# Optimization experiments

Measured on AMD Instinct MI355X. Metric: run time of the kernel, lower is better.

The kernel has to match this reference:

```python
import jax, jax.numpy as jnp
import numpy as np

TAPS, DIMS, SPS = 32, 2, 2
LR_W, LR_F, LR_S, LR_B = 1.0 / 2**6, 1.0 / 2**7, 0.0, 1.0 / 2**11
GRAD_MAX_W, GRAD_MAX_F = 30.0, 30.0
EPS, BETA = 1e-8, 0.0


def _const16qam():
    # commplax comm.const('16QAM', norm=True): unit-average-power 16QAM grid
    p = np.array([-3.0, -1.0, 1.0, 3.0], dtype=np.float32)
    c = (p[:, None] + 1j * p[None, :]).reshape(-1) / np.sqrt(10.0)
    return jnp.asarray(c, dtype=jnp.complex64)


def _frame(x, flen, fstep):
    # xop.frame: [L, D] -> [(L-flen)//fstep + 1, flen, D]
    n = (x.shape[0] - flen) // fstep + 1
    idx = jnp.arange(n)[:, None] * fstep + jnp.arange(flen)[None, :]
    return x[idx]


def _clip(g, gmax):
    # same math as jnp.where(|g|>gmax, g/|g|*gmax, g), but NaN-safe under AD
    ag = jnp.abs(g)
    return g * jnp.minimum(1.0, gmax / jnp.maximum(ag, 1e-30))


def _ddlms(x):
    const = _const16qam()
    u_all = _frame(x, TAPS, SPS)  # [N, taps, dims] complex64

    def step(state, u):
        w, f, s, b, fshat = state
        v = jnp.einsum('ijt,tj->i', w, u)          # mimo filter output [dims]
        k = v * f
        c = k * s
        z = c + b
        q = v * fshat + b
        # decision-directed symbol (train=False, no truth)
        d = const[jnp.argmin(jnp.abs(const[:, None] - q[None, :]), axis=0)]
        psi_hat = jnp.abs(f) / f * jnp.abs(s) / s
        e_w = (d - b) * psi_hat - v
        e_f = d - b - k
        e_s = d - b - c
        e_b = d - z
        gw = -1.0 / ((jnp.abs(u) ** 2).sum() + EPS) * e_w[:, None, None] * u.conj().T[None, ...]
        gf = -1.0 / (jnp.abs(v) ** 2 + EPS) * e_f * v.conj()
        gs = -1.0 / (jnp.abs(k) ** 2 + EPS) * e_s * k.conj()
        gb = -e_b
        gw = _clip(gw, GRAD_MAX_W)
        gf = _clip(gf, GRAD_MAX_F)
        out = (w, f, s, b)  # pre-update params are used by apply
        wn = w - LR_W * gw
        fn = f - LR_F * gf
        sn = s - LR_S * gs
        bn = b - LR_B * gb
        fshatn = BETA * fshat + (1.0 - BETA) * (fn * sn)
        return (wn, fn, sn, bn, fshatn), out

    dt = jnp.complex64
    state0 = (jnp.zeros((DIMS, DIMS, TAPS), dt),   # w0 (mimoinit='zeros')
              jnp.ones((DIMS,), dt),               # f0
              jnp.ones((DIMS,), dt),               # s0
              jnp.zeros((DIMS,), dt),              # b0
              jnp.ones((DIMS,), dt))               # fshat0
    _, (ws, fs, ss, bs) = jax.lax.scan(step, state0, u_all)
    # mimo_apply: vmap(mimo)(ws, u_all) * fs * ss + bs
    y = jnp.einsum('nijt,ntj->ni', ws, u_all) * fs * ss + bs  # [N, dims]
    return y


def setup_inputs() -> dict:
    key = jax.random.key(0)
    k1, k2 = jax.random.split(key)
    x_re = jax.random.normal(k1, (200000, 2), dtype=jnp.float32)
    x_im = jax.random.normal(k2, (200000, 2), dtype=jnp.float32)
    return {"x_re": x_re, "x_im": x_im}


def reference(x_re, x_im):
    x = jax.lax.complex(x_re, x_im)  # [2N, 2] complex64
    y = _ddlms(x)                    # [(2N-taps)//sps + 1, 2] complex64
    return jnp.stack([y.real, y.imag], axis=-1)  # [N_out, 2, 2] float32
```

## Files before the change

### kernel.cpp

```cpp
#include <hip/hip_runtime.h>

typedef unsigned u2v __attribute__((ext_vector_type(2)));

template<int CTRL>
__device__ __forceinline__ float dpp_xadd(float v) {
    int s = __builtin_amdgcn_update_dpp(0, __float_as_int(v), CTRL, 0xF, 0xF, true);
    return v + __int_as_float(s);
}

#if __has_builtin(__builtin_amdgcn_permlane16_swap)
__device__ __forceinline__ float xor16_add(float v) {
    u2v r = __builtin_amdgcn_permlane16_swap((unsigned)__float_as_int(v),
                                             (unsigned)__float_as_int(v),
                                             false, false);
    return __int_as_float((int)r.x) + __int_as_float((int)r.y);
}
#else
__device__ __forceinline__ float xor16_add(float v) {
    int s = __builtin_amdgcn_ds_swizzle(__float_as_int(v), 0x401F);
    return v + __int_as_float(s);
}
#endif

__device__ __forceinline__ float red32(float v) {
    v = dpp_xadd<0xB1>(v);
    v = dpp_xadd<0x4E>(v);
    v = dpp_xadd<0x141>(v);
    v = dpp_xadd<0x140>(v);
    v = xor16_add(v);
    return v;
}

__global__ void pre_tab(const float* __restrict__ xre,
                        const float* __restrict__ xim,
                        float4* __restrict__ tab, int ns) {
    int n = blockIdx.x * blockDim.x + threadIdx.x;
    if (n >= ns) return;
    const float* ar = xre + 4 * n;
    const float* ai = xim + 4 * n;
    float un = 0.f;
    #pragma unroll 8
    for (int k = 0; k < 64; ++k) un = fmaf(ar[k], ar[k], fmaf(ai[k], ai[k], un));
    float s = (1.0f / 64.0f) / (un + 1e-8f);
    float cr = 0.f, ci = 0.f;
    if (n + 1 < ns) {
        const float* br_ = ar + 4;
        const float* bi_ = ai + 4;
        #pragma unroll 8
        for (int k = 0; k < 64; ++k) {
            cr = fmaf(ar[k], br_[k], fmaf(ai[k], bi_[k], cr));
            ci = fmaf(ar[k], bi_[k], ci);
            ci = fmaf(-ai[k], br_[k], ci);
        }
    }
    tab[n] = make_float4(s, s * cr, s * ci, 0.f);
}

#define NSTEPS 99985

__global__ __launch_bounds__(128, 1)
void ddlms_scan2(const float* __restrict__ xre,
                 const float* __restrict__ xim,
                 const float4* __restrict__ tab,
                 float* __restrict__ out) {
    const int tid = (int)threadIdx.x;
    const int wid = tid >> 6;
    const int l = tid & 63;
    const int m = l & 31;
    const int half = l >> 5;

    constexpr float EPSv = 1e-8f;
    constexpr float LRF  = 1.0f / 128.0f;
    constexpr float LRB  = 1.0f / 2048.0f;
    const float B1 = 0.6324555320336759f;
    const float A1 = 0.31622776601683794f;
    const float A3 = 0.9486832980505138f;

    __shared__ float2 sh[8];
    if (tid < 8) sh[tid] = make_float2(0.f, 0.f);
    __syncthreads();

    float2* __restrict__ o2 = reinterpret_cast<float2*>(out);

    if (wid == 0) {
        float fr = 1.f, fi = 0.f, br = 0.f, bi = 0.f, psr = 1.f, psj = 0.f;
        float ewPr = 0.f, ewPi = 0.f, sCPr = 0.f, sCPi = 0.f;
        float4 t0 = tab[0], t1 = tab[1], t2 = tab[2], t3;

        auto W0 = [&](int n, int P, float4& tC, float4& tF) {
            __syncthreads();
            float2 bas = sh[2 * P + half];
            float Dr = fmaf(ewPr, sCPr, -(ewPi * sCPi));
            float Di = fmaf(ewPr, sCPi,   ewPi * sCPr);
            float vr = bas.x + Dr, vi = bas.y + Di;
            { int nn = n + 3; if (nn > NSTEPS - 1) nn = NSTEPS - 1; tF = tab[nn]; }

            float kr = fmaf(vr, fr, -(vi * fi));
            float ki = fmaf(vr, fi,   vi * fr);
            float zr = kr + br, zi = ki + bi;
            if (m == 0) o2[2 * n + half] = make_float2(zr, zi);

            float magr = (fabsf(zr) > B1) ? A3 : A1;
            float dr   = (zr <= 0.f) ? -magr : magr;
            float magi = (fabsf(zi) > B1) ? A3 : A1;
            float di   = (zi <= 0.f) ? -magi : magi;

            float er = dr - zr, ei = di - zi;

            float v2  = fmaf(vr, vr, fmaf(vi, vi, EPSv));
            float rv  = __builtin_amdgcn_rcpf(v2);
            float gfr = fmaf(er, vr,   ei * vi)  * rv;
            float gfi = fmaf(ei, vr, -(er * vi)) * rv;
            float m2  = fmaf(gfr, gfr, gfi * gfi);
            float scf = fminf(1.f, 30.f * __builtin_amdgcn_rsqf(m2));
            float tf  = LRF * scf;

            float dbr = dr - br, dbi = di - bi;
            float ewr = fmaf(dbr, psr, -(dbi * psj)) - vr;
            float ewi = fmaf(dbr, psj,   dbi * psr)  - vi;

            float ewsr = tC.x * ewr, ewsi = tC.x * ewi;
            if (m == 0) sh[4 + 2 * P + half] = make_float2(ewsr, ewsi);

            fr = fmaf(tf, gfr, fr); fi = fmaf(tf, gfi, fi);
            br = fmaf(LRB, er, br); bi = fmaf(LRB, ei, bi);

            float ff = fmaf(fr, fr, fi * fi);
            float rs = __builtin_amdgcn_rsqf(ff);
            psr = fr * rs; psj = -(fi * rs);

            ewPr = ewr; ewPi = ewi; sCPr = tC.y; sCPi = tC.z;
        };

        int n = 0;
        for (int it = 0; it < 24996; ++it) {
            W0(n + 0, 0, t0, t3);
            W0(n + 1, 1, t1, t0);
            W0(n + 2, 0, t2, t1);
            W0(n + 3, 1, t3, t2);
            n += 4;
        }
        W0(99984, 0, t0, t3);
    } else {
        float wAr = 0.f, wAi = 0.f, wBr = 0.f, wBi = 0.f;

        auto LOADU = [&](int nn, float& a, float& b_, float& c, float& d_) {
            const float* pr = xre + 4 * nn;
            const float* pi = xim + 4 * nn;
            a = pr[m]; c = pr[m + 32]; b_ = pi[m]; d_ = pi[m + 32];
        };

        float u0Ar, u0Ai, u0Br, u0Bi, u1Ar, u1Ai, u1Br, u1Bi,
              u2Ar, u2Ai, u2Br, u2Bi, u3Ar, u3Ai, u3Br, u3Bi;
        u3Ar = u3Ai = u3Br = u3Bi = 0.f;
        LOADU(0, u0Ar, u0Ai, u0Br, u0Bi);
        LOADU(1, u1Ar, u1Ai, u1Br, u1Bi);
        LOADU(2, u2Ar, u2Ai, u2Br, u2Bi);

        auto W1 = [&](int n, int P,
            float& uPAr, float& uPAi, float& uPBr, float& uPBi,
            float& uNAr, float& uNAi, float& uNBr, float& uNBi) {
            __syncthreads();
            float2 ews = sh[4 + 2 * (1 - P) + half];
            wAr = fmaf(ews.x, uPAr, fmaf( ews.y, uPAi, wAr));
            wAi = fmaf(ews.y, uPAr, fmaf(-ews.x, uPAi, wAi));
            wBr = fmaf(ews.x, uPBr, fmaf( ews.y, uPBi, wBr));
            wBi = fmaf(ews.y, uPBr, fmaf(-ews.x, uPBi, wBi));
            { int nn = n + 3; if (nn > NSTEPS - 1) nn = NSTEPS - 1;
              LOADU(nn, uPAr, uPAi, uPBr, uPBi); }
            float prr = wAr * uNAr; prr = fmaf(-wAi, uNAi, prr);
            prr = fmaf(wBr, uNBr, prr); prr = fmaf(-wBi, uNBi, prr);
            float pri = wAr * uNAi; pri = fmaf( wAi, uNAr, pri);
            pri = fmaf(wBr, uNBi, pri); pri = fmaf( wBi, uNBr, pri);
            float basr = red32(prr), basi = red32(pri);
            if (m == 0) sh[2 * (1 - P) + half] = make_float2(basr, basi);
        };

        int n = 0;
        for (int it = 0; it < 24996; ++it) {
            W1(n + 0, 0, u3Ar,u3Ai,u3Br,u3Bi, u1Ar,u1Ai,u1Br,u1Bi);
            W1(n + 1, 1, u0Ar,u0Ai,u0Br,u0Bi, u2Ar,u2Ai,u2Br,u2Bi);
            W1(n + 2, 0, u1Ar,u1Ai,u1Br,u1Bi, u3Ar,u3Ai,u3Br,u3Bi);
            W1(n + 3, 1, u2Ar,u2Ai,u2Br,u2Bi, u0Ar,u0Ai,u0Br,u0Bi);
            n += 4;
        }
        W1(99984, 0, u3Ar,u3Ai,u3Br,u3Bi, u1Ar,u1Ai,u1Br,u1Bi);
    }
}

__global__ __launch_bounds__(64, 1)
void ddlms_scan_fb(const float* __restrict__ xre,
                   const float* __restrict__ xim,
                   float* __restrict__ out) {
    const int l = (int)threadIdx.x;
    const int m = l & 31;
    const int half = l >> 5;
    constexpr float EPSv = 1e-8f;
    constexpr float LRW  = 1.0f / 64.0f;
    constexpr float LRF  = 1.0f / 128.0f;
    constexpr float LRB  = 1.0f / 2048.0f;
    const float B1 = 0.6324555320336759f;
    const float A1 = 0.31622776601683794f;
    const float A3 = 0.9486832980505138f;
    float wAr=0.f, wAi=0.f, wBr=0.f, wBi=0.f;
    float fr=1.f, fi=0.f, br=0.f, bi=0.f, psr=1.f, psj=0.f;
    float vr=0.f, vi=0.f, ewPr=0.f, ewPi=0.f, sP=0.f;
    float2* __restrict__ o2 = reinterpret_cast<float2*>(out);
    auto LOADU = [&](int nn, float& a, float& b_, float& c, float& d_) {
        const float* pr = xre + 4 * nn;
        const float* pi = xim + 4 * nn;
        a = pr[m]; c = pr[m + 32]; b_ = pi[m]; d_ = pi[m + 32];
    };
    float pAr,pAi,pBr,pBi, qAr,qAi,qBr,qBi, rAr,rAi,rBr,rBi;
    pAr=pAi=pBr=pBi=0.f;
    LOADU(0, qAr,qAi,qBr,qBi);
    LOADU(1, rAr,rAi,rBr,rBi);
    auto STEP = [&](int n,
        float& uPAr, float& uPAi, float& uPBr, float& uPBi,
        float& uCAr, float& uCAi, float& uCBr, float& uCBi,
        float& uNAr, float& uNAi, float& uNBr, float& uNBi) {
        {
            float gr = ewPr * uPAr; gr = fmaf( ewPi, uPAi, gr);
            float gi = ewPi * uPAr; gi = fmaf(-ewPr, uPAi, gi);
            wAr = fmaf(sP, gr, wAr); wAi = fmaf(sP, gi, wAi);
            float hr = ewPr * uPBr; hr = fmaf( ewPi, uPBi, hr);
            float hi = ewPi * uPBr; hi = fmaf(-ewPr, uPBi, hi);
            wBr = fmaf(sP, hr, wBr); wBi = fmaf(sP, hi, wBi);
        }
        float basr, basi;
        {
            float prr = wAr * uNAr; prr = fmaf(-wAi, uNAi, prr);
            prr = fmaf(wBr, uNBr, prr); prr = fmaf(-wBi, uNBi, prr);
            float pri = wAr * uNAi; pri = fmaf( wAi, uNAr, pri);
            pri = fmaf(wBr, uNBi, pri); pri = fmaf( wBi, uNBr, pri);
            basr = red32(prr); basi = red32(pri);
        }
        float uu = uCAr*uCAr; uu = fmaf(uCAi,uCAi,uu);
        uu = fmaf(uCBr,uCBr,uu); uu = fmaf(uCBi,uCBi,uu);
        float sN = LRW * __builtin_amdgcn_rcpf(red32(uu) + EPSv);
        float ccr = uCAr*uNAr; ccr = fmaf(uCAi,uNAi,ccr);
        ccr = fmaf(uCBr,uNBr,ccr); ccr = fmaf(uCBi,uNBi,ccr);
        float cci = uCAr*uNAi; cci = fmaf(-uCAi,uNAr,cci);
        cci = fmaf(uCBr,uNBi,cci); cci = fmaf(-uCBi,uNBr,cci);
        float sCr = sN * red32(ccr), sCi = sN * red32(cci);
        float kr = fmaf(vr, fr, -(vi * fi));
        float ki = fmaf(vr, fi,   vi * fr);
        float zr = kr + br, zi = ki + bi;
        if (m == 0) o2[2 * n + half] = make_float2(zr, zi);
        float magr = (fabsf(zr) > B1) ? A3 : A1;
        float dr   = (zr <= 0.f) ? -magr : magr;
        float magi = (fabsf(zi) > B1) ? A3 : A1;
        float di   = (zi <= 0.f) ? -magi : magi;
        float er = dr - zr, ei = di - zi;
        float v2  = fmaf(vr, vr, fmaf(vi, vi, EPSv));
        float rv  = __builtin_amdgcn_rcpf(v2);
        float gfr = fmaf(er, vr,   ei * vi)  * rv;
        float gfi = fmaf(ei, vr, -(er * vi)) * rv;
        float m2  = fmaf(gfr, gfr, gfi * gfi);
        float scf = fminf(1.f, 30.f * __builtin_amdgcn_rsqf(m2));
        float tf  = LRF * scf;
        float dbr = dr - br, dbi = di - bi;
        float ewr = fmaf(dbr, psr, -(dbi * psj)) - vr;
        float ewi = fmaf(dbr, psj,   dbi * psr)  - vi;
        float Dr = fmaf(ewr, sCr, -(ewi * sCi));
        float Di = fmaf(ewr, sCi,   ewi * sCr);
        vr = basr + Dr; vi = basi + Di;
        fr = fmaf(tf, gfr, fr); fi = fmaf(tf, gfi, fi);
        br = fmaf(LRB, er, br); bi = fmaf(LRB, ei, bi);
        float ff = fmaf(fr, fr, fi * fi);
        float rs = __builtin_amdgcn_rsqf(ff);
        psr = fr * rs; psj = -(fi * rs);
        ewPr = ewr; ewPi = ewi; sP = sN;
        int nn = n + 2; if (nn > NSTEPS - 1) nn = NSTEPS - 1;
        LOADU(nn, uPAr, uPAi, uPBr, uPBi);
    };
    int n = 0;
    for (int it = 0; it < 33328; ++it) {
        STEP(n,     pAr,pAi,pBr,pBi,  qAr,qAi,qBr,qBi,  rAr,rAi,rBr,rBi);
        STEP(n + 1, qAr,qAi,qBr,qBi,  rAr,rAi,rBr,rBi,  pAr,pAi,pBr,pBi);
        STEP(n + 2, rAr,rAi,rBr,rBi,  pAr,pAi,pBr,pBi,  qAr,qAi,qBr,qBi);
        n += 3;
    }
    STEP(99984, pAr,pAi,pBr,pBi, qAr,qAi,qBr,qBi, rAr,rAi,rBr,rBi);
}

extern "C" void kernel_launch(void* const* d_in, const int* in_sizes, int n_in,
                              void* d_out, int out_size, void* d_ws, size_t ws_size,
                              hipStream_t stream) {
    const float* xre = (const float*)d_in[0];
    const float* xim = (const float*)d_in[1];
    float* out = (float*)d_out;
    const int NS = NSTEPS;

    if (ws_size >= (size_t)NS * sizeof(float4)) {
        float4* tab = (float4*)d_ws;
        pre_tab<<<(NS + 255) / 256, 256, 0, stream>>>(xre, xim, tab, NS);
        ddlms_scan2<<<1, 128, 0, stream>>>(xre, xim, tab, out);
    } else {
        ddlms_scan_fb<<<1, 64, 0, stream>>>(xre, xim, out);
    }
}
```

Before: 19.63 ms.

## Widen scan lookahead to three steps with pairwise barriers between waves

The precompute kernel now stores, for each step, the input correlation against the previous three steps as well as the normalizer. The scalar wave can then fold the last three error terms into the filter output locally and only needs to sync with the weight-update wave every two steps instead of every step. The weight wave applies two rank-one updates and produces two base outputs per barrier. This halves the number of block-wide barriers on the serial critical path, in exchange for more per-step FMAs, a workspace table twice as large, and more bookkeeping in the pipelined recurrence.

```diff
diff --git a/kernel.cpp b/kernel.cpp
--- a/kernel.cpp
+++ b/kernel.cpp
@@ -1,13 +1,14 @@
 #include <hip/hip_runtime.h>
 
 typedef unsigned u2v __attribute__((ext_vector_type(2)));
+
+#define NS 99985
 
 template<int CTRL>
 __device__ __forceinline__ float dpp_xadd(float v) {
     int s = __builtin_amdgcn_update_dpp(0, __float_as_int(v), CTRL, 0xF, 0xF, true);
     return v + __int_as_float(s);
 }
-
 #if __has_builtin(__builtin_amdgcn_permlane16_swap)
 __device__ __forceinline__ float xor16_add(float v) {
     u2v r = __builtin_amdgcn_permlane16_swap((unsigned)__float_as_int(v),
@@ -21,19 +22,15 @@
     return v + __int_as_float(s);
 }
 #endif
-
 __device__ __forceinline__ float red32(float v) {
-    v = dpp_xadd<0xB1>(v);
-    v = dpp_xadd<0x4E>(v);
-    v = dpp_xadd<0x141>(v);
-    v = dpp_xadd<0x140>(v);
-    v = xor16_add(v);
-    return v;
-}
-
-__global__ void pre_tab(const float* __restrict__ xre,
-                        const float* __restrict__ xim,
-                        float4* __restrict__ tab, int ns) {
+    v = dpp_xadd<0xB1>(v); v = dpp_xadd<0x4E>(v);
+    v = dpp_xadd<0x141>(v); v = dpp_xadd<0x140>(v);
+    return xor16_add(v);
+}
+
+__global__ void pre_tab8(const float* __restrict__ xre,
+                         const float* __restrict__ xim,
+                         float4* __restrict__ tab8, int ns) {
     int n = blockIdx.x * blockDim.x + threadIdx.x;
     if (n >= ns) return;
     const float* ar = xre + 4 * n;
@@ -42,26 +39,30 @@
     #pragma unroll 8
     for (int k = 0; k < 64; ++k) un = fmaf(ar[k], ar[k], fmaf(ai[k], ai[k], un));
     float s = (1.0f / 64.0f) / (un + 1e-8f);
-    float cr = 0.f, ci = 0.f;
-    if (n + 1 < ns) {
-        const float* br_ = ar + 4;
-        const float* bi_ = ai + 4;
-        #pragma unroll 8
-        for (int k = 0; k < 64; ++k) {
-            cr = fmaf(ar[k], br_[k], fmaf(ai[k], bi_[k], cr));
-            ci = fmaf(ar[k], bi_[k], ci);
-            ci = fmaf(-ai[k], br_[k], ci);
-        }
+    float C[3][2];
+    #pragma unroll
+    for (int j = 1; j <= 3; ++j) {
+        float cr = 0.f, ci = 0.f;
+        if (n >= j) {
+            const float* pr = ar - 4 * j;
+            const float* pi = ai - 4 * j;
+            #pragma unroll 8
+            for (int k = 0; k < 64; ++k) {
+                cr = fmaf(pr[k], ar[k], fmaf(pi[k], ai[k], cr));
+                ci = fmaf(pr[k], ai[k], ci);
+                ci = fmaf(-pi[k], ar[k], ci);
+            }
+        }
+        C[j - 1][0] = cr; C[j - 1][1] = ci;
     }
-    tab[n] = make_float4(s, s * cr, s * ci, 0.f);
-}
-
-#define NSTEPS 99985
+    tab8[2 * n]     = make_float4(s, C[0][0], C[0][1], 0.f);
+    tab8[2 * n + 1] = make_float4(C[1][0], C[1][1], C[2][0], C[2][1]);
+}
 
 __global__ __launch_bounds__(128, 1)
-void ddlms_scan2(const float* __restrict__ xre,
+void ddlms_scan3(const float* __restrict__ xre,
                  const float* __restrict__ xim,
-                 const float4* __restrict__ tab,
+                 const float4* __restrict__ tab8,
                  float* __restrict__ out) {
     const int tid = (int)threadIdx.x;
     const int wid = tid >> 6;
@@ -76,24 +77,26 @@
     const float A1 = 0.31622776601683794f;
     const float A3 = 0.9486832980505138f;
 
-    __shared__ float2 sh[8];
-    if (tid < 8) sh[tid] = make_float2(0.f, 0.f);
+    __shared__ float2 sh[16];
+    if (tid < 16) sh[tid] = make_float2(0.f, 0.f);
     __syncthreads();
 
     float2* __restrict__ o2 = reinterpret_cast<float2*>(out);
 
     if (wid == 0) {
         float fr = 1.f, fi = 0.f, br = 0.f, bi = 0.f, psr = 1.f, psj = 0.f;
-        float ewPr = 0.f, ewPi = 0.f, sCPr = 0.f, sCPi = 0.f;
-        float4 t0 = tab[0], t1 = tab[1], t2 = tab[2], t3;
-
-        auto W0 = [&](int n, int P, float4& tC, float4& tF) {
-            __syncthreads();
-            float2 bas = sh[2 * P + half];
-            float Dr = fmaf(ewPr, sCPr, -(ewPi * sCPi));
-            float Di = fmaf(ewPr, sCPi,   ewPi * sCPr);
-            float vr = bas.x + Dr, vi = bas.y + Di;
-            { int nn = n + 3; if (nn > NSTEPS - 1) nn = NSTEPS - 1; tF = tab[nn]; }
+        float e1r = 0.f, e1i = 0.f, e2r = 0.f, e2i = 0.f, e3r = 0.f, e3i = 0.f;
+
+        auto CSTEP = [&](int n, int Q, int j, const float4& tA, const float4& tB,
+                         bool tail) {
+            float2 B = sh[4 * Q + 2 * j + half];
+            float vr = B.x, vi = B.y;
+            vr = fmaf(e1r, tA.y, vr); vr = fmaf(-e1i, tA.z, vr);
+            vi = fmaf(e1r, tA.z, vi); vi = fmaf( e1i, tA.y, vi);
+            vr = fmaf(e2r, tB.x, vr); vr = fmaf(-e2i, tB.y, vr);
+            vi = fmaf(e2r, tB.y, vi); vi = fmaf( e2i, tB.x, vi);
+            vr = fmaf(e3r, tB.z, vr); vr = fmaf(-e3i, tB.w, vr);
+            vi = fmaf(e3r, tB.w, vi); vi = fmaf( e3i, tB.z, vi);
 
             float kr = fmaf(vr, fr, -(vi * fi));
             float ki = fmaf(vr, fi,   vi * fr);
@@ -119,72 +122,101 @@
             float ewr = fmaf(dbr, psr, -(dbi * psj)) - vr;
             float ewi = fmaf(dbr, psj,   dbi * psr)  - vi;
 
-            float ewsr = tC.x * ewr, ewsi = tC.x * ewi;
-            if (m == 0) sh[4 + 2 * P + half] = make_float2(ewsr, ewsi);
+            if (!tail) {
+                float ewsr = tA.x * ewr, ewsi = tA.x * ewi;
+                if (m == 0) sh[8 + 4 * Q + 2 * j + half] = make_float2(ewsr, ewsi);
+                e3r = e2r; e3i = e2i; e2r = e1r; e2i = e1i; e1r = ewsr; e1i = ewsi;
+            }
 
             fr = fmaf(tf, gfr, fr); fi = fmaf(tf, gfi, fi);
             br = fmaf(LRB, er, br); bi = fmaf(LRB, ei, bi);
-
             float ff = fmaf(fr, fr, fi * fi);
             float rs = __builtin_amdgcn_rsqf(ff);
             psr = fr * rs; psj = -(fi * rs);
-
-            ewPr = ewr; ewPi = ewi; sCPr = tC.y; sCPi = tC.z;
         };
+
+        auto PREF = [&](int n0, float4& a0, float4& b0, float4& a1, float4& b1) {
+            int na = n0;     if (na > NS - 1) na = NS - 1;
+            int nb = n0 + 1; if (nb > NS - 1) nb = NS - 1;
+            a0 = tab8[2 * na]; b0 = tab8[2 * na + 1];
+            a1 = tab8[2 * nb]; b1 = tab8[2 * nb + 1];
+        };
+
+        float4 cA0 = tab8[0], cB0 = tab8[1], cA1 = tab8[2], cB1 = tab8[3];
+        float4 nA0, nB0, nA1, nB1;
 
         int n = 0;
         for (int it = 0; it < 24996; ++it) {
-            W0(n + 0, 0, t0, t3);
-            W0(n + 1, 1, t1, t0);
-            W0(n + 2, 0, t2, t1);
-            W0(n + 3, 1, t3, t2);
+            CSTEP(n,     0, 0, cA0, cB0, false);
+            CSTEP(n + 1, 0, 1, cA1, cB1, false);
+            PREF(n + 2, nA0, nB0, nA1, nB1);
+            __syncthreads();
+            CSTEP(n + 2, 1, 0, nA0, nB0, false);
+            CSTEP(n + 3, 1, 1, nA1, nB1, false);
+            PREF(n + 4, cA0, cB0, cA1, cB1);
+            __syncthreads();
             n += 4;
         }
-        W0(99984, 0, t0, t3);
+        CSTEP(99984, 0, 0, cA0, cB0, true);
     } else {
         float wAr = 0.f, wAi = 0.f, wBr = 0.f, wBi = 0.f;
 
         auto LOADU = [&](int nn, float& a, float& b_, float& c, float& d_) {
+            if (nn > NS - 1) nn = NS - 1;
             const float* pr = xre + 4 * nn;
             const float* pi = xim + 4 * nn;
             a = pr[m]; c = pr[m + 32]; b_ = pi[m]; d_ = pi[m + 32];
         };
 
-        float u0Ar, u0Ai, u0Br, u0Bi, u1Ar, u1Ai, u1Br, u1Bi,
-              u2Ar, u2Ai, u2Br, u2Bi, u3Ar, u3Ai, u3Br, u3Bi;
-        u3Ar = u3Ai = u3Br = u3Bi = 0.f;
-        LOADU(0, u0Ar, u0Ai, u0Br, u0Bi);
-        LOADU(1, u1Ar, u1Ai, u1Br, u1Bi);
-        LOADU(2, u2Ar, u2Ai, u2Br, u2Bi);
-
-        auto W1 = [&](int n, int P,
-            float& uPAr, float& uPAi, float& uPBr, float& uPBi,
-            float& uNAr, float& uNAi, float& uNBr, float& uNBi) {
-            __syncthreads();
-            float2 ews = sh[4 + 2 * (1 - P) + half];
-            wAr = fmaf(ews.x, uPAr, fmaf( ews.y, uPAi, wAr));
-            wAi = fmaf(ews.y, uPAr, fmaf(-ews.x, uPAi, wAi));
-            wBr = fmaf(ews.x, uPBr, fmaf( ews.y, uPBi, wBr));
-            wBi = fmaf(ews.y, uPBr, fmaf(-ews.x, uPBi, wBi));
-            { int nn = n + 3; if (nn > NSTEPS - 1) nn = NSTEPS - 1;
-              LOADU(nn, uPAr, uPAi, uPBr, uPBi); }
-            float prr = wAr * uNAr; prr = fmaf(-wAi, uNAi, prr);
-            prr = fmaf(wBr, uNBr, prr); prr = fmaf(-wBi, uNBi, prr);
-            float pri = wAr * uNAi; pri = fmaf( wAi, uNAr, pri);
-            pri = fmaf(wBr, uNBi, pri); pri = fmaf( wBi, uNBr, pri);
-            float basr = red32(prr), basi = red32(pri);
-            if (m == 0) sh[2 * (1 - P) + half] = make_float2(basr, basi);
+        float p0[8], p1[8], p2[8];
+        #pragma unroll
+        for (int q = 0; q < 8; ++q) p0[q] = 0.f;
+        LOADU(0, p1[0], p1[1], p1[2], p1[3]);
+        LOADU(1, p1[4], p1[5], p1[6], p1[7]);
+        LOADU(2, p2[0], p2[1], p2[2], p2[3]);
+        LOADU(3, p2[4], p2[5], p2[6], p2[7]);
+
+        auto PSTEP = [&](int n2k, int Q, float* W, float* Bp) {
+            float2 ea = sh[8 + 4 * (1 - Q) + 0 + half];
+            float2 eb = sh[8 + 4 * (1 - Q) + 2 + half];
+            wAr = fmaf(ea.x, W[0], fmaf( ea.y, W[1], wAr));
+            wAi = fmaf(ea.y, W[0], fmaf(-ea.x, W[1], wAi));
+            wBr = fmaf(ea.x, W[2], fmaf( ea.y, W[3], wBr));
+            wBi = fmaf(ea.y, W[2], fmaf(-ea.x, W[3], wBi));
+            {
+                float prr = wAr * Bp[0]; prr = fmaf(-wAi, Bp[1], prr);
+                prr = fmaf(wBr, Bp[2], prr); prr = fmaf(-wBi, Bp[3], prr);
+                float pri = wAr * Bp[1]; pri = fmaf( wAi, Bp[0], pri);
+                pri = fmaf(wBr, Bp[3], pri); pri = fmaf( wBi, Bp[2], pri);
+                float basr = red32(prr), basi = red32(pri);
+                if (m == 0) sh[4 * (1 - Q) + 0 + half] = make_float2(basr, basi);
+            }
+            wAr = fmaf(eb.x, W[4], fmaf( eb.y, W[5], wAr));
+            wAi = fmaf(eb.y, W[4], fmaf(-eb.x, W[5], wAi));
+            wBr = fmaf(eb.x, W[6], fmaf( eb.y, W[7], wBr));
+            wBi = fmaf(eb.y, W[6], fmaf(-eb.x, W[7], wBi));
+            {
+                float prr = wAr * Bp[4]; prr = fmaf(-wAi, Bp[5], prr);
+                prr = fmaf(wBr, Bp[6], prr); prr = fmaf(-wBi, Bp[7], prr);
+                float pri = wAr * Bp[5]; pri = fmaf( wAi, Bp[4], pri);
+                pri = fmaf(wBr, Bp[7], pri); pri = fmaf( wBi, Bp[6], pri);
+                float basr = red32(prr), basi = red32(pri);
+                if (m == 0) sh[4 * (1 - Q) + 2 + half] = make_float2(basr, basi);
+            }
+            LOADU(n2k + 4, W[0], W[1], W[2], W[3]);
+            LOADU(n2k + 5, W[4], W[5], W[6], W[7]);
         };
 
-        int n = 0;
-        for (int it = 0; it < 24996; ++it) {
-            W1(n + 0, 0, u3Ar,u3Ai,u3Br,u3Bi, u1Ar,u1Ai,u1Br,u1Bi);
-            W1(n + 1, 1, u0Ar,u0Ai,u0Br,u0Bi, u2Ar,u2Ai,u2Br,u2Bi);
-            W1(n + 2, 0, u1Ar,u1Ai,u1Br,u1Bi, u3Ar,u3Ai,u3Br,u3Bi);
-            W1(n + 3, 1, u2Ar,u2Ai,u2Br,u2Bi, u0Ar,u0Ai,u0Br,u0Bi);
-            n += 4;
-        }
-        W1(99984, 0, u3Ar,u3Ai,u3Br,u3Bi, u1Ar,u1Ai,u1Br,u1Bi);
+        int n0 = 0;
+        for (int i = 0; i < 8332; ++i) {
+            PSTEP(n0,      0, p0, p2); __syncthreads();
+            PSTEP(n0 + 2,  1, p1, p0); __syncthreads();
+            PSTEP(n0 + 4,  0, p2, p1); __syncthreads();
+            PSTEP(n0 + 6,  1, p0, p2); __syncthreads();
+            PSTEP(n0 + 8,  0, p1, p0); __syncthreads();
+            PSTEP(n0 + 10, 1, p2, p1); __syncthreads();
+            n0 += 12;
+        }
     }
 }
 
@@ -271,7 +303,7 @@
         float rs = __builtin_amdgcn_rsqf(ff);
         psr = fr * rs; psj = -(fi * rs);
         ewPr = ewr; ewPi = ewi; sP = sN;
-        int nn = n + 2; if (nn > NSTEPS - 1) nn = NSTEPS - 1;
+        int nn = n + 2; if (nn > NS - 1) nn = NS - 1;
         LOADU(nn, uPAr, uPAi, uPBr, uPBi);
     };
     int n = 0;
@@ -290,12 +322,11 @@
     const float* xre = (const float*)d_in[0];
     const float* xim = (const float*)d_in[1];
     float* out = (float*)d_out;
-    const int NS = NSTEPS;
-
-    if (ws_size >= (size_t)NS * sizeof(float4)) {
-        float4* tab = (float4*)d_ws;
-        pre_tab<<<(NS + 255) / 256, 256, 0, stream>>>(xre, xim, tab, NS);
-        ddlms_scan2<<<1, 128, 0, stream>>>(xre, xim, tab, out);
+
+    if (ws_size >= (size_t)2 * NS * sizeof(float4)) {
+        float4* tab8 = (float4*)d_ws;
+        pre_tab8<<<(NS + 255) / 256, 256, 0, stream>>>(xre, xim, tab8, NS);
+        ddlms_scan3<<<1, 128, 0, stream>>>(xre, xim, tab8, out);
     } else {
         ddlms_scan_fb<<<1, 64, 0, stream>>>(xre, xim, out);
     }
```

After: 28.28 ms. 44.0% more time.
